# Kernel optimization log

Hardware: AMD Instinct MI355X
Metric: run time of the kernel (lower is better)

The kernel has to match this reference:

```python
import jax, jax.numpy as jnp
import numpy as np

NUM_USER = 100000
K = 32
DIM = 64

def setup_inputs() -> dict:
    key = jax.random.key(0)
    k1, k2, k3 = jax.random.split(key, 3)
    features = jax.random.normal(k1, (NUM_USER, DIM), dtype=jnp.float32)
    user_graph = jax.random.randint(k2, (NUM_USER, K), 0, NUM_USER, dtype=jnp.int64)
    user_matrix = jax.random.uniform(k3, (NUM_USER, K), dtype=jnp.float32)
    return {"features": features, "user_graph": user_graph, "user_matrix": user_matrix}

def reference(features, user_graph, user_matrix):
    # u_features: [num_user, k, dim] gather of neighbor features
    u_features = features[user_graph]
    # weighted sum over k neighbors: [num_user, k] x [num_user, k, dim] -> [num_user, dim]
    u_pre = jnp.einsum('nk,nkd->nd', user_matrix, u_features)
    return u_pre
```

## Files before the change

kernel.cpp:

```cpp
#include <hip/hip_runtime.h>
#include <hip/hip_bf16.h>

#define NUM_USER 100000
#define K_NEIGH 32
#define DIM 64

typedef float floatx2 __attribute__((ext_vector_type(2)));
typedef float floatx4 __attribute__((ext_vector_type(4)));
typedef unsigned int uintx2 __attribute__((ext_vector_type(2)));

__global__ __launch_bounds__(256) void convert_bf16_kernel(
    const floatx2* __restrict__ feat2,
    unsigned int*  __restrict__ table) {
  int i = blockIdx.x * blockDim.x + threadIdx.x;
  if (i >= NUM_USER * DIM / 2) return;
  floatx2 f = feat2[i];
  unsigned int ux = __float_as_uint(f.x);
  unsigned int uy = __float_as_uint(f.y);
  unsigned int bx = (ux + 0x7fffu + ((ux >> 16) & 1u)) >> 16;
  unsigned int by = (uy + 0x7fffu + ((uy >> 16) & 1u)) >> 16;
  table[i] = bx | (by << 16);
}

__global__ __launch_bounds__(256) void user_graph_gather_bf16_kernel(
    const uintx2* __restrict__ table2,
    const int*    __restrict__ graph,
    const float*  __restrict__ matrix,
    floatx4*      __restrict__ out4) {
  int t  = blockIdx.x * blockDim.x + threadIdx.x;
  int u  = t >> 4;
  int d4 = t & 15;
  if (u >= NUM_USER) return;

  const int*   g = graph  + u * K_NEIGH;
  const float* w = matrix + u * K_NEIGH;

  float a0 = 0.f, a1 = 0.f, a2 = 0.f, a3 = 0.f;
#pragma unroll
  for (int k = 0; k < K_NEIGH; ++k) {
    int   idx = g[k];
    float wk  = w[k];
    uintx2 p  = table2[idx * 16 + d4];
    float f0 = __uint_as_float(p.x << 16);
    float f1 = __uint_as_float(p.x & 0xffff0000u);
    float f2 = __uint_as_float(p.y << 16);
    float f3 = __uint_as_float(p.y & 0xffff0000u);
    a0 += wk * f0;
    a1 += wk * f1;
    a2 += wk * f2;
    a3 += wk * f3;
  }
  floatx4 r; r.x = a0; r.y = a1; r.z = a2; r.w = a3;
  out4[u * 16 + d4] = r;
}

__global__ __launch_bounds__(256) void user_graph_gather_f32_kernel(
    const float* __restrict__ features,
    const int*   __restrict__ graph,
    const float* __restrict__ matrix,
    float*       __restrict__ out) {
  int t = blockIdx.x * blockDim.x + threadIdx.x;
  int u = t >> 6;
  int d = t & 63;
  if (u >= NUM_USER) return;
  const int*   g = graph  + (size_t)u * K_NEIGH;
  const float* w = matrix + (size_t)u * K_NEIGH;
  float acc = 0.f;
#pragma unroll
  for (int k = 0; k < K_NEIGH; ++k)
    acc += w[k] * features[(size_t)g[k] * DIM + d];
  out[(size_t)u * DIM + d] = acc;
}

extern "C" void kernel_launch(void* const* d_in, const int* in_sizes, int n_in,
                              void* d_out, int out_size, void* d_ws, size_t ws_size,
                              hipStream_t stream) {
  const float* features = (const float*)d_in[0];
  const int*   graph    = (const int*)d_in[1];
  const float* matrix   = (const float*)d_in[2];

  const size_t table_bytes = (size_t)NUM_USER * DIM * 2;
  if (ws_size >= table_bytes) {
    unsigned int* table = (unsigned int*)d_ws;
    const int n_pack = NUM_USER * DIM / 2;
    convert_bf16_kernel<<<(n_pack + 255) / 256, 256, 0, stream>>>(
        (const floatx2*)features, table);
    const int total = NUM_USER * 16;
    user_graph_gather_bf16_kernel<<<(total + 255) / 256, 256, 0, stream>>>(
        (const uintx2*)table, graph, matrix, (floatx4*)d_out);
  } else {
    const int total = NUM_USER * DIM;
    user_graph_gather_f32_kernel<<<(total + 255) / 256, 256, 0, stream>>>(
        features, graph, matrix, (float*)d_out);
  }
}
```

Measured before the change: 140.6 us.

## Presort neighbor indices per user and pack index-weight pairs before gather

Adds a pre-pass kernel that bitonic-sorts each user's 32 neighbor indices with their weights and writes packed (index, weight) pairs to workspace. The gather kernel then reads one 8-byte pair per neighbor instead of two separate loads, and visits feature rows in ascending address order. The aim is better cache locality and fewer scalar loads in the gather. The cost is an extra kernel launch, heavy per-thread register use for the sort, and about 25 MB of extra workspace traffic. Summation order changes slightly.

```diff
diff --git a/kernel.cpp b/kernel.cpp
--- a/kernel.cpp
+++ b/kernel.cpp
@@ -22,7 +22,72 @@
   table[i] = bx | (by << 16);
 }
 
+__global__ __launch_bounds__(256) void sort_pairs_kernel(
+    const int*   __restrict__ graph,
+    const float* __restrict__ matrix,
+    uintx2*      __restrict__ pairs) {
+  int u = blockIdx.x * blockDim.x + threadIdx.x;
+  if (u >= NUM_USER) return;
+  const int*   g = graph  + u * K_NEIGH;
+  const float* w = matrix + u * K_NEIGH;
+  int   idx[K_NEIGH];
+  float wv[K_NEIGH];
+#pragma unroll
+  for (int k = 0; k < K_NEIGH; ++k) { idx[k] = g[k]; wv[k] = w[k]; }
+#pragma unroll
+  for (int k = 2; k <= K_NEIGH; k <<= 1) {
+#pragma unroll
+    for (int j = k >> 1; j > 0; j >>= 1) {
+#pragma unroll
+      for (int i = 0; i < K_NEIGH; ++i) {
+        int l = i ^ j;
+        if (l > i) {
+          bool up = ((i & k) == 0);
+          bool sw = up ? (idx[i] > idx[l]) : (idx[i] < idx[l]);
+          int   ti = sw ? idx[l] : idx[i];
+          int   tl = sw ? idx[i] : idx[l];
+          float si = sw ? wv[l]  : wv[i];
+          float sl = sw ? wv[i]  : wv[l];
+          idx[i] = ti; idx[l] = tl; wv[i] = si; wv[l] = sl;
+        }
+      }
+    }
+  }
+#pragma unroll
+  for (int k = 0; k < K_NEIGH; ++k) {
+    uintx2 p; p.x = (unsigned int)idx[k]; p.y = __float_as_uint(wv[k]);
+    pairs[u * K_NEIGH + k] = p;
+  }
+}
+
 __global__ __launch_bounds__(256) void user_graph_gather_bf16_kernel(
+    const uintx2* __restrict__ table2,
+    const uintx2* __restrict__ pairs,
+    floatx4*      __restrict__ out4) {
+  int t  = blockIdx.x * blockDim.x + threadIdx.x;
+  int u  = t >> 4;
+  int d4 = t & 15;
+  if (u >= NUM_USER) return;
+
+  const uintx2* pp = pairs + u * K_NEIGH;
+
+  float a0 = 0.f, a1 = 0.f, a2 = 0.f, a3 = 0.f;
+#pragma unroll
+  for (int k = 0; k < K_NEIGH; ++k) {
+    uintx2 p  = pp[k];
+    int    idx = (int)p.x;
+    float  wk  = __uint_as_float(p.y);
+    uintx2 f  = table2[idx * 16 + d4];
+    a0 += wk * __uint_as_float(f.x << 16);
+    a1 += wk * __uint_as_float(f.x & 0xffff0000u);
+    a2 += wk * __uint_as_float(f.y << 16);
+    a3 += wk * __uint_as_float(f.y & 0xffff0000u);
+  }
+  floatx4 r; r.x = a0; r.y = a1; r.z = a2; r.w = a3;
+  out4[u * 16 + d4] = r;
+}
+
+__global__ __launch_bounds__(256) void gather_bf16_nosort_kernel(
     const uintx2* __restrict__ table2,
     const int*    __restrict__ graph,
     const float*  __restrict__ matrix,
@@ -31,24 +96,18 @@
   int u  = t >> 4;
   int d4 = t & 15;
   if (u >= NUM_USER) return;
-
   const int*   g = graph  + u * K_NEIGH;
   const float* w = matrix + u * K_NEIGH;
-
   float a0 = 0.f, a1 = 0.f, a2 = 0.f, a3 = 0.f;
 #pragma unroll
   for (int k = 0; k < K_NEIGH; ++k) {
     int   idx = g[k];
     float wk  = w[k];
-    uintx2 p  = table2[idx * 16 + d4];
-    float f0 = __uint_as_float(p.x << 16);
-    float f1 = __uint_as_float(p.x & 0xffff0000u);
-    float f2 = __uint_as_float(p.y << 16);
-    float f3 = __uint_as_float(p.y & 0xffff0000u);
-    a0 += wk * f0;
-    a1 += wk * f1;
-    a2 += wk * f2;
-    a3 += wk * f3;
+    uintx2 f  = table2[idx * 16 + d4];
+    a0 += wk * __uint_as_float(f.x << 16);
+    a1 += wk * __uint_as_float(f.x & 0xffff0000u);
+    a2 += wk * __uint_as_float(f.y << 16);
+    a3 += wk * __uint_as_float(f.y & 0xffff0000u);
   }
   floatx4 r; r.x = a0; r.y = a1; r.z = a2; r.w = a3;
   out4[u * 16 + d4] = r;
@@ -80,13 +139,27 @@
   const float* matrix   = (const float*)d_in[2];
 
   const size_t table_bytes = (size_t)NUM_USER * DIM * 2;
-  if (ws_size >= table_bytes) {
+  const size_t pairs_bytes = (size_t)NUM_USER * K_NEIGH * 8;
+
+  if (ws_size >= table_bytes + pairs_bytes) {
+    unsigned int* table = (unsigned int*)d_ws;
+    uintx2*       pairs = (uintx2*)((char*)d_ws + table_bytes);
+
+    const int n_pack = NUM_USER * DIM / 2;
+    convert_bf16_kernel<<<(n_pack + 255) / 256, 256, 0, stream>>>(
+        (const floatx2*)features, table);
+    sort_pairs_kernel<<<(NUM_USER + 255) / 256, 256, 0, stream>>>(
+        graph, matrix, pairs);
+    const int total = NUM_USER * 16;
+    user_graph_gather_bf16_kernel<<<(total + 255) / 256, 256, 0, stream>>>(
+        (const uintx2*)table, (const uintx2*)pairs, (floatx4*)d_out);
+  } else if (ws_size >= table_bytes) {
     unsigned int* table = (unsigned int*)d_ws;
     const int n_pack = NUM_USER * DIM / 2;
     convert_bf16_kernel<<<(n_pack + 255) / 256, 256, 0, stream>>>(
         (const floatx2*)features, table);
     const int total = NUM_USER * 16;
-    user_graph_gather_bf16_kernel<<<(total + 255) / 256, 256, 0, stream>>>(
+    gather_bf16_nosort_kernel<<<(total + 255) / 256, 256, 0, stream>>>(
         (const uintx2*)table, graph, matrix, (floatx4*)d_out);
   } else {
     const int total = NUM_USER * DIM;
```

After: 338.8 us. +140.9%, slower.
